# Kernel tuning notes

Measured on AMD Instinct MI355X. Metric: run time of the kernel, lower is better.

## Reference

```python
import jax, jax.numpy as jnp
import numpy as np

B, IN, D, E, K = 16384, 2048, 1024, 3, 2
H1, H2 = 1024, 512


def setup_inputs() -> dict:
    key = jax.random.key(0)
    ks = jax.random.split(key, 10)
    x = jax.random.normal(ks[0], (B, IN), dtype=jnp.float32)
    gate = jax.random.normal(ks[1], (B, E), dtype=jnp.float32)
    topk_probs = jax.random.uniform(ks[2], (B, K), dtype=jnp.float32)
    topk_idx = jax.random.randint(ks[3], (B, K), 0, E)
    s = 0.02
    W1 = jax.random.normal(ks[4], (E, IN, H1), dtype=jnp.float32) * s
    b1 = jnp.zeros((E, H1), dtype=jnp.float32)
    W2 = jax.random.normal(ks[5], (E, H1, H2), dtype=jnp.float32) * s
    b2 = jnp.zeros((E, H2), dtype=jnp.float32)
    W3 = jax.random.normal(ks[6], (E, H2, D), dtype=jnp.float32) * s
    b3 = jnp.zeros((E, D), dtype=jnp.float32)
    return {"x": x, "gate": gate, "topk_probs": topk_probs, "topk_idx": topk_idx,
            "W1": W1, "b1": b1, "W2": W2, "b2": b2, "W3": W3, "b3": b3}


def _lrelu(v):
    return jnp.where(v > 0, v, 0.2 * v)  # LeakyReLU(0.2)


def reference(x, gate, topk_probs, topk_idx, W1, b1, W2, b2, W3, b3):
    # gate is accepted by the original forward but never used.
    n_experts = W1.shape[0]
    # Per-expert 3-layer MLP, batched over experts: [E, B, *]
    h = _lrelu(jnp.einsum('bi,eio->ebo', x, W1) + b1[:, None, :])
    h = _lrelu(jnp.einsum('ebi,eio->ebo', h, W2) + b2[:, None, :])
    y = jnp.einsum('ebi,eio->ebo', h, W3) + b3[:, None, :]  # [E, B, D]
    # Combine: weight for expert e on token b = sum_k probs[b,k] * [idx[b,k]==e]
    onehot = topk_idx[None, :, :] == jnp.arange(n_experts)[:, None, None]  # [E,B,K]
    w = jnp.sum(jnp.where(onehot, topk_probs[None, :, :], 0.0), axis=-1)  # [E,B]
    return jnp.einsum('eb,ebd->bd', w, y)
```

## Files before the change

kernel.cpp:

```cpp
#include <hip/hip_runtime.h>
#include <cstdint>
#include <cstddef>

#define B_TOK   16384
#define IN_DIM  2048
#define D_DIM   1024
#define NEXP    3
#define TOPK    2
#define H1_DIM  1024
#define H2_DIM  512

typedef __bf16 bf16x8 __attribute__((ext_vector_type(8)));
typedef float  f32x4  __attribute__((ext_vector_type(4)));
typedef unsigned short ushort8_t __attribute__((ext_vector_type(8)));

__device__ __forceinline__ unsigned short f2bf(float f) {
    unsigned int u = __builtin_bit_cast(unsigned int, f);
    return (unsigned short)((u + 0x7fffu + ((u >> 16) & 1u)) >> 16);
}
__device__ __forceinline__ float bf2f(unsigned short v) {
    return __builtin_bit_cast(float, (unsigned int)v << 16);
}

__device__ __forceinline__ void glds16(const void* gsrc, void* ldst) {
    __builtin_amdgcn_global_load_lds(
        (__attribute__((address_space(1))) void*)(gsrc),
        (__attribute__((address_space(3))) void*)(ldst),
        16, 0, 0);
}

__global__ __launch_bounds__(256) void prepass(
    const float* __restrict__ x, unsigned short* __restrict__ xb,
    const float* __restrict__ W1s, const float* __restrict__ W2s,
    const float* __restrict__ W3s,
    unsigned short* __restrict__ W1d, unsigned short* __restrict__ W2d,
    unsigned short* __restrict__ W3d,
    const float* __restrict__ probs, const int* __restrict__ tidx,
    int* __restrict__ cnt, int* __restrict__ list, int* __restrict__ inv)
{
    const int bid = blockIdx.x;
    const int t = threadIdx.x;

    if (bid < 2048) {
        const size_t n = (size_t)B_TOK * IN_DIM;
        const size_t stride = (size_t)2048 * 256 * 8;
        size_t i = ((size_t)bid * 256 + t) * 8;
        for (; i < n; i += stride) {
            float4 a = *(const float4*)(x + i);
            float4 b = *(const float4*)(x + i + 4);
            ushort8_t o;
            o[0] = f2bf(a.x); o[1] = f2bf(a.y); o[2] = f2bf(a.z); o[3] = f2bf(a.w);
            o[4] = f2bf(b.x); o[5] = f2bf(b.y); o[6] = f2bf(b.z); o[7] = f2bf(b.w);
            *(ushort8_t*)(xb + i) = o;
        }
    } else if (bid < 4352) {
        __shared__ unsigned short tile[64][68];
        int r = (bid - 2048) % 768;
        int e = (bid - 2048) / 768;
        const float* W; unsigned short* Wt; int K, N, tx;
        if (r < 512)      { W = W1s; Wt = W1d; K = IN_DIM; N = H1_DIM; tx = r; }
        else if (r < 640) { W = W2s; Wt = W2d; K = H1_DIM; N = H2_DIM; tx = r - 512; }
        else              { W = W3s; Wt = W3d; K = H2_DIM; N = D_DIM;  tx = r - 640; }
        const int ntx = N >> 6;
        const float* Wp = W + (size_t)e * K * N;
        unsigned short* Wtp = Wt + (size_t)e * N * K;
        int n0 = (tx % ntx) * 64, k0 = (tx / ntx) * 64;
        int nn = (t & 15) * 4;
        int kk = t >> 4;
        #pragma unroll
        for (int rr = 0; rr < 4; ++rr) {
            int k = kk + rr * 16;
            float4 v = *(const float4*)(Wp + (size_t)(k0 + k) * N + (n0 + nn));
            tile[k][nn + 0] = f2bf(v.x);
            tile[k][nn + 1] = f2bf(v.y);
            tile[k][nn + 2] = f2bf(v.z);
            tile[k][nn + 3] = f2bf(v.w);
        }
        __syncthreads();
        int n  = t >> 2;
        int kb = (t & 3) * 16;
        ushort8_t o0, o1;
        #pragma unroll
        for (int i = 0; i < 8; ++i) o0[i] = tile[kb + i][n];
        #pragma unroll
        for (int i = 0; i < 8; ++i) o1[i] = tile[kb + 8 + i][n];
        unsigned short* dst = Wtp + (size_t)(n0 + n) * K + (k0 + kb);
        *(ushort8_t*)dst = o0;
        *(ushort8_t*)(dst + 8) = o1;
    } else {
        __shared__ int lcnt[NEXP];
        __shared__ int lbase[NEXP];
        __shared__ int ltok[NEXP][256];
        int b = (bid - 4352) * 256 + t;
        if (t < NEXP) lcnt[t] = 0;
        __syncthreads();
        int i0 = tidx[b * TOPK + 0], i1 = tidx[b * TOPK + 1];
        #pragma unroll
        for (int e = 0; e < NEXP; ++e) {
            if (i0 == e || i1 == e) {
                int s = atomicAdd(&lcnt[e], 1);
                ltok[e][s] = b;
            }
        }
        __syncthreads();
        if (t < NEXP) lbase[t] = atomicAdd(&cnt[t], lcnt[t]);
        __syncthreads();
        #pragma unroll
        for (int e = 0; e < NEXP; ++e) {
            int n = lcnt[e], base = lbase[e];
            for (int s = t; s < n; s += 256) {
                int tk = ltok[e][s];
                list[e * B_TOK + base + s] = tk;
                inv[e * B_TOK + tk] = base + s;
            }
        }
    }
}

__global__ __launch_bounds__(256) void combine_out(
    const float* __restrict__ probs, const int* __restrict__ tidx,
    const int* __restrict__ inv, const unsigned short* __restrict__ y, size_t ypl,
    float* __restrict__ out)
{
    int gid = blockIdx.x * 256 + threadIdx.x;
    int tok = gid >> 7;
    int dc  = (gid & 127) << 3;
    float p0 = probs[tok * TOPK + 0], p1 = probs[tok * TOPK + 1];
    int   i0 = tidx [tok * TOPK + 0], i1 = tidx [tok * TOPK + 1];
    size_t r0 = (size_t)i0 * ypl + (size_t)inv[(size_t)i0 * B_TOK + tok] * D_DIM + dc;
    size_t r1 = (size_t)i1 * ypl + (size_t)inv[(size_t)i1 * B_TOK + tok] * D_DIM + dc;
    ushort8_t a = *(const ushort8_t*)(y + r0);
    ushort8_t b = *(const ushort8_t*)(y + r1);
    float4 o0, o1;
    o0.x = p0 * bf2f(a[0]) + p1 * bf2f(b[0]);
    o0.y = p0 * bf2f(a[1]) + p1 * bf2f(b[1]);
    o0.z = p0 * bf2f(a[2]) + p1 * bf2f(b[2]);
    o0.w = p0 * bf2f(a[3]) + p1 * bf2f(b[3]);
    o1.x = p0 * bf2f(a[4]) + p1 * bf2f(b[4]);
    o1.y = p0 * bf2f(a[5]) + p1 * bf2f(b[5]);
    o1.z = p0 * bf2f(a[6]) + p1 * bf2f(b[6]);
    o1.w = p0 * bf2f(a[7]) + p1 * bf2f(b[7]);
    float* op = out + (size_t)tok * D_DIM + dc;
    *(float4*)op = o0;
    *(float4*)(op + 4) = o1;
}

template<int ACT, int GATHER>
__global__ __launch_bounds__(512, 2) void gemm8(
    const unsigned short* __restrict__ Ab, size_t Aplane,
    const unsigned short* __restrict__ Bb,
    const float* __restrict__ biasb,
    unsigned short* __restrict__ Hb,
    size_t plane,
    const int* __restrict__ listb,
    const int* __restrict__ cntb,
    int N, int K, int NT, int e0)
{
    const int bid  = blockIdx.x;
    const int xcd  = bid & 7;
    const int slot = bid >> 3;
    const int q    = slot / NT;
    const int nt   = slot % NT;
    const int ti   = q * 8 + xcd;
    const int e    = e0 + (ti >> 6);
    const int mt   = ti & 63;
    const int bm   = mt << 8;
    const int cp   = (cntb[e] + 255) & ~255;
    if (bm >= cp) return;
    const int bn   = nt << 8;

    __shared__ char smem[131072];

    const int tid  = threadIdx.x;
    const int lane = tid & 63;
    const int w    = tid >> 6;
    const int wl3  = w & 3;
    const int wn1  = w >> 2;
    const int l15  = lane & 15;
    const int ug8  = (((tid & 7) ^ ((tid >> 3) & 7)) << 3);
    const int sw0  = ((((lane >> 4) + 0) ^ (lane & 7)) << 4);
    const int sw1  = ((((lane >> 4) + 4) ^ (lane & 7)) << 4);

    const int* listp = listb + (size_t)e * B_TOK;
    const unsigned short* Ae = Ab + (size_t)e * Aplane;
    const unsigned short* Be = Bb + (size_t)e * ((size_t)N * K);
    const float* biasp = biasb + (size_t)e * N;

    const unsigned short* sA[2][2];
    const unsigned short* sB[2][2];
    #pragma unroll
    for (int h = 0; h < 2; ++h)
        #pragma unroll
        for (int j = 0; j < 2; ++j) {
            int lrow = h * 128 + j * 64 + (tid >> 3);
            int arow;
            if constexpr (GATHER) arow = listp[bm + lrow];
            else                  arow = bm + lrow;
            sA[h][j] = Ae + (size_t)arow * K + ug8;
            sB[h][j] = Be + (size_t)(bn + lrow) * K + ug8;
        }

    char* const stA = smem + (w << 10);
    char* const stB = smem + 65536 + (w << 10);
    const char* const rA = smem + (wl3 * 32 + l15) * 128;
    const char* const rB = smem + 65536 + (wn1 * 64 + l15) * 128;

    f32x4 acc[2][2][2][4] = {};
    bf16x8 av[2][2];
    bf16x8 bv[4][2];

#define STA(db, h, kt) do {                                                     \
    glds16(sA[h][0] + (size_t)(kt) * 64, stA + (db) * 32768 + (h) * 16384);     \
    glds16(sA[h][1] + (size_t)(kt) * 64, stA + (db) * 32768 + (h) * 16384 + 8192); } while (0)
#define STB(db, h, kt) do {                                                     \
    glds16(sB[h][0] + (size_t)(kt) * 64, stB + (db) * 32768 + (h) * 16384);     \
    glds16(sB[h][1] + (size_t)(kt) * 64, stB + (db) * 32768 + (h) * 16384 + 8192); } while (0)

#define LAk(db, Qm, kk) do {                                                    \
    _Pragma("unroll")                                                           \
    for (int ml = 0; ml < 2; ++ml)                                              \
        av[ml][kk] = *(const bf16x8*)(rA + (db)*32768 + (Qm)*16384 + ml*2048    \
                                      + ((kk) ? sw1 : sw0));                    \
    } while (0)
#define LBk(db, Qn, kk) do {                                                    \
    _Pragma("unroll")                                                           \
    for (int nl = 0; nl < 4; ++nl)                                              \
        bv[nl][kk] = *(const bf16x8*)(rB + (db)*32768 + (Qn)*16384 + nl*2048    \
                                      + ((kk) ? sw1 : sw0));                    \
    } while (0)

#define GK(Qm, Qn, kk) do {                                                     \
    _Pragma("unroll")                                                           \
    for (int ml = 0; ml < 2; ++ml)                                              \
        _Pragma("unroll")                                                       \
        for (int nl = 0; nl < 4; ++nl)                                          \
            acc[Qm][ml][Qn][nl] = __builtin_amdgcn_mfma_f32_16x16x32_bf16(      \
                av[ml][kk], bv[nl][kk], acc[Qm][ml][Qn][nl], 0, 0, 0);          \
    } while (0)

#define WINDOW(Qm, Qn, STAGE_STMT, VM_STMT, LK0, LK1) do {                      \
    STAGE_STMT;                                                                 \
    VM_STMT;                                                                    \
    __builtin_amdgcn_s_setprio(1);                                              \
    GK(Qm, Qn, 0);                                                              \
    __builtin_amdgcn_sched_barrier(0);                                          \
    LK0;                                                                        \
    __builtin_amdgcn_sched_barrier(0);                                          \
    GK(Qm, Qn, 1);                                                              \
    __builtin_amdgcn_sched_barrier(0);                                          \
    LK1;                                                                        \
    __builtin_amdgcn_s_setprio(0);                                              \
    __builtin_amdgcn_sched_barrier(0);                                          \
    __builtin_amdgcn_s_barrier();                                               \
} while (0)

    const int nkt = K >> 6;
    STA(0, 0, 0); STA(0, 1, 0); STB(0, 0, 0); STB(0, 1, 0);
    STA(1, 0, 1); STB(1, 0, 1);
    asm volatile("s_waitcnt vmcnt(4)" ::: "memory");
    __builtin_amdgcn_s_barrier();
    LAk(0, 1, 0); LAk(0, 1, 1); LBk(0, 0, 0); LBk(0, 0, 1);

    const int niter = nkt >> 1;
    for (int it = 0; it < niter; ++it) {
        const int t1 = 2 * it + 1;
        const int t2 = (2 * it + 2 < nkt) ? 2 * it + 2 : nkt - 1;
        const int t3 = (2 * it + 3 < nkt) ? 2 * it + 3 : nkt - 1;
        WINDOW(1, 0, STA(1, 1, t1), ((void)0), LAk(0, 0, 0), LAk(0, 0, 1));
        WINDOW(0, 0, STB(1, 1, t1), ((void)0), LBk(0, 1, 0), LBk(0, 1, 1));
        WINDOW(0, 1, STA(0, 0, t2), ((void)0), LAk(0, 1, 0), LAk(0, 1, 1));
        WINDOW(1, 1, STB(0, 0, t2),
               asm volatile("s_waitcnt vmcnt(4)" ::: "memory"),
               LAk(1, 1, 0); LBk(1, 0, 0), LAk(1, 1, 1); LBk(1, 0, 1));
        WINDOW(1, 0, STA(0, 1, t2), ((void)0), LAk(1, 0, 0), LAk(1, 0, 1));
        WINDOW(0, 0, STB(0, 1, t2), ((void)0), LBk(1, 1, 0), LBk(1, 1, 1));
        WINDOW(0, 1, STA(1, 0, t3), ((void)0), LAk(1, 1, 0), LAk(1, 1, 1));
        WINDOW(1, 1, STB(1, 0, t3),
               asm volatile("s_waitcnt vmcnt(4)" ::: "memory"),
               LAk(0, 1, 0); LBk(0, 0, 0), LAk(0, 1, 1); LBk(0, 0, 1));
    }
    asm volatile("s_waitcnt vmcnt(0)" ::: "memory");

    const int rl = (lane >> 4) << 2;
    float bsv[2][4];
    #pragma unroll
    for (int Qn = 0; Qn < 2; ++Qn)
        #pragma unroll
        for (int nl = 0; nl < 4; ++nl)
            bsv[Qn][nl] = biasp[bn + Qn * 128 + wn1 * 64 + nl * 16 + l15];

    unsigned short* Hp = Hb + (size_t)e * plane;
    #pragma unroll
    for (int Qm = 0; Qm < 2; ++Qm)
    #pragma unroll
    for (int ml = 0; ml < 2; ++ml)
    #pragma unroll
    for (int jj = 0; jj < 4; ++jj) {
        int srow = bm + Qm * 128 + wl3 * 32 + ml * 16 + rl + jj;
        size_t ro = (size_t)srow * N;
        #pragma unroll
        for (int Qn = 0; Qn < 2; ++Qn)
        #pragma unroll
        for (int nl = 0; nl < 4; ++nl) {
            int col = bn + Qn * 128 + wn1 * 64 + nl * 16 + l15;
            float v = acc[Qm][ml][Qn][nl][jj] + bsv[Qn][nl];
            if (ACT) v = v > 0.f ? v : 0.2f * v;
            Hp[ro + col] = f2bf(v);
        }
    }
#undef WINDOW
#undef GK
#undef LAk
#undef LBk
#undef STA
#undef STB
}


extern "C" void kernel_launch(void* const* d_in, const int* in_sizes, int n_in,
                              void* d_out, int out_size, void* d_ws, size_t ws_size,
                              hipStream_t stream)
{
    const float* x     = (const float*)d_in[0];
    const float* probs = (const float*)d_in[2];
    const int*   tidx  = (const int*)d_in[3];
    const float* W1    = (const float*)d_in[4];
    const float* b1    = (const float*)d_in[5];
    const float* W2    = (const float*)d_in[6];
    const float* b2    = (const float*)d_in[7];
    const float* W3    = (const float*)d_in[8];
    const float* b3    = (const float*)d_in[9];
    float* out = (float*)d_out;

    char* ws = (char*)d_ws;
    const size_t xb_off  = 0;
    const size_t w1t_off = xb_off  + (size_t)B_TOK * IN_DIM * 2;
    const size_t w2t_off = w1t_off + (size_t)NEXP * IN_DIM * H1_DIM * 2;
    const size_t w3t_off = w2t_off + (size_t)NEXP * H1_DIM * H2_DIM * 2;
    const size_t h1_off  = w3t_off + (size_t)NEXP * H2_DIM * D_DIM * 2;
    const size_t h2_off  = h1_off  + (size_t)NEXP * B_TOK * H1_DIM * 2;
    const size_t y_off   = h2_off  + (size_t)NEXP * B_TOK * H2_DIM * 2;
    const size_t li_off  = y_off   + (size_t)NEXP * B_TOK * D_DIM * 2;
    const size_t cn_off  = li_off  + (size_t)NEXP * B_TOK * 4;
    const size_t iv_off  = cn_off  + 256;

    unsigned short* xb  = (unsigned short*)(ws + xb_off);
    unsigned short* W1t = (unsigned short*)(ws + w1t_off);
    unsigned short* W2t = (unsigned short*)(ws + w2t_off);
    unsigned short* W3t = (unsigned short*)(ws + w3t_off);
    unsigned short* h1  = (unsigned short*)(ws + h1_off);
    unsigned short* h2  = (unsigned short*)(ws + h2_off);
    unsigned short* y   = (unsigned short*)(ws + y_off);
    int*            lst = (int*)(ws + li_off);
    int*            cnt = (int*)(ws + cn_off);
    int*            inv = (int*)(ws + iv_off);

    hipMemsetAsync(lst, 0, (size_t)NEXP * B_TOK * 4 + 256, stream);

    prepass<<<4416, 256, 0, stream>>>(x, xb, W1, W2, W3, W1t, W2t, W3t,
                                      probs, tidx, cnt, lst, inv);

    const size_t h1pl = (size_t)B_TOK * H1_DIM;
    const size_t h2pl = (size_t)B_TOK * H2_DIM;
    const size_t ypl  = (size_t)B_TOK * D_DIM;

    gemm8<1, 1><<<dim3(NEXP * 64 * 4), 512, 0, stream>>>(
        xb, 0, W1t, b1, h1, h1pl,
        lst, cnt, H1_DIM, IN_DIM, 4, 0);
    gemm8<1, 0><<<dim3(NEXP * 64 * 2), 512, 0, stream>>>(
        h1, h1pl, W2t, b2, h2, h2pl,
        lst, cnt, H2_DIM, H1_DIM, 2, 0);
    gemm8<0, 0><<<dim3(NEXP * 64 * 4), 512, 0, stream>>>(
        h2, h2pl, W3t, b3, y, ypl,
        lst, cnt, D_DIM, H2_DIM, 4, 0);
    combine_out<<<dim3(B_TOK * 128 / 256), 256, 0, stream>>>(
        probs, tidx, inv, y, ypl, out);
}
```

Before: 276.6 us.

## Move W2/W3 bf16 transposes from prepass into extra blocks of first GEMM

The prepass now only converts x and W1 and builds the routing lists. The W2 and W3 bf16 transposes run in 384 extra 512-thread blocks appended to the layer-1 GEMM launch, two 256-thread tiles per block. The aim is to shorten the serial prepass and overlap the weight conversion with GEMM1's tail or idle CUs. The cost is that those extra blocks reserve 128KB of shared memory each, so they compete with GEMM tiles for CU slots, and the grid scheduling order decides whether they actually overlap.

```diff
diff --git a/kernel.cpp b/kernel.cpp
--- a/kernel.cpp
+++ b/kernel.cpp
@@ -29,13 +29,38 @@
         16, 0, 0);
 }
 
+__device__ __forceinline__ void transpose_tile_256(
+    const float* __restrict__ Wp, unsigned short* __restrict__ Wtp,
+    int K, int N, int n0, int k0, int t, unsigned short (*tile)[68])
+{
+    int nn = (t & 15) * 4;
+    int kk = t >> 4;
+    #pragma unroll
+    for (int rr = 0; rr < 4; ++rr) {
+        int k = kk + rr * 16;
+        float4 v = *(const float4*)(Wp + (size_t)(k0 + k) * N + (n0 + nn));
+        tile[k][nn + 0] = f2bf(v.x);
+        tile[k][nn + 1] = f2bf(v.y);
+        tile[k][nn + 2] = f2bf(v.z);
+        tile[k][nn + 3] = f2bf(v.w);
+    }
+    __syncthreads();
+    int n  = t >> 2;
+    int kb = (t & 3) * 16;
+    ushort8_t o0, o1;
+    #pragma unroll
+    for (int i = 0; i < 8; ++i) o0[i] = tile[kb + i][n];
+    #pragma unroll
+    for (int i = 0; i < 8; ++i) o1[i] = tile[kb + 8 + i][n];
+    unsigned short* dst = Wtp + (size_t)(n0 + n) * K + (k0 + kb);
+    *(ushort8_t*)dst = o0;
+    *(ushort8_t*)(dst + 8) = o1;
+}
+
 __global__ __launch_bounds__(256) void prepass(
     const float* __restrict__ x, unsigned short* __restrict__ xb,
-    const float* __restrict__ W1s, const float* __restrict__ W2s,
-    const float* __restrict__ W3s,
-    unsigned short* __restrict__ W1d, unsigned short* __restrict__ W2d,
-    unsigned short* __restrict__ W3d,
-    const float* __restrict__ probs, const int* __restrict__ tidx,
+    const float* __restrict__ W1s, unsigned short* __restrict__ W1d,
+    const int* __restrict__ tidx,
     int* __restrict__ cnt, int* __restrict__ list, int* __restrict__ inv)
 {
     const int bid = blockIdx.x;
@@ -53,45 +78,21 @@
             o[4] = f2bf(b.x); o[5] = f2bf(b.y); o[6] = f2bf(b.z); o[7] = f2bf(b.w);
             *(ushort8_t*)(xb + i) = o;
         }
-    } else if (bid < 4352) {
+    } else if (bid < 3584) {
         __shared__ unsigned short tile[64][68];
-        int r = (bid - 2048) % 768;
-        int e = (bid - 2048) / 768;
-        const float* W; unsigned short* Wt; int K, N, tx;
-        if (r < 512)      { W = W1s; Wt = W1d; K = IN_DIM; N = H1_DIM; tx = r; }
-        else if (r < 640) { W = W2s; Wt = W2d; K = H1_DIM; N = H2_DIM; tx = r - 512; }
-        else              { W = W3s; Wt = W3d; K = H2_DIM; N = D_DIM;  tx = r - 640; }
-        const int ntx = N >> 6;
-        const float* Wp = W + (size_t)e * K * N;
-        unsigned short* Wtp = Wt + (size_t)e * N * K;
-        int n0 = (tx % ntx) * 64, k0 = (tx / ntx) * 64;
-        int nn = (t & 15) * 4;
-        int kk = t >> 4;
-        #pragma unroll
-        for (int rr = 0; rr < 4; ++rr) {
-            int k = kk + rr * 16;
-            float4 v = *(const float4*)(Wp + (size_t)(k0 + k) * N + (n0 + nn));
-            tile[k][nn + 0] = f2bf(v.x);
-            tile[k][nn + 1] = f2bf(v.y);
-            tile[k][nn + 2] = f2bf(v.z);
-            tile[k][nn + 3] = f2bf(v.w);
-        }
-        __syncthreads();
-        int n  = t >> 2;
-        int kb = (t & 3) * 16;
-        ushort8_t o0, o1;
-        #pragma unroll
-        for (int i = 0; i < 8; ++i) o0[i] = tile[kb + i][n];
-        #pragma unroll
-        for (int i = 0; i < 8; ++i) o1[i] = tile[kb + 8 + i][n];
-        unsigned short* dst = Wtp + (size_t)(n0 + n) * K + (k0 + kb);
-        *(ushort8_t*)dst = o0;
-        *(ushort8_t*)(dst + 8) = o1;
+        int g = bid - 2048;
+        int e = g / 512;
+        int r = g % 512;
+        const int ntx = H1_DIM >> 6;
+        int n0 = (r % ntx) * 64, k0 = (r / ntx) * 64;
+        transpose_tile_256(W1s + (size_t)e * IN_DIM * H1_DIM,
+                           W1d + (size_t)e * H1_DIM * IN_DIM,
+                           IN_DIM, H1_DIM, n0, k0, t, tile);
     } else {
         __shared__ int lcnt[NEXP];
         __shared__ int lbase[NEXP];
         __shared__ int ltok[NEXP][256];
-        int b = (bid - 4352) * 256 + t;
+        int b = (bid - 3584) * 256 + t;
         if (t < NEXP) lcnt[t] = 0;
         __syncthreads();
         int i0 = tidx[b * TOPK + 0], i1 = tidx[b * TOPK + 1];
@@ -145,7 +146,7 @@
     *(float4*)(op + 4) = o1;
 }
 
-template<int ACT, int GATHER>
+template<int ACT, int GATHER, int XTRA>
 __global__ __launch_bounds__(512, 2) void gemm8(
     const unsigned short* __restrict__ Ab, size_t Aplane,
     const unsigned short* __restrict__ Bb,
@@ -154,9 +155,32 @@
     size_t plane,
     const int* __restrict__ listb,
     const int* __restrict__ cntb,
-    int N, int K, int NT, int e0)
+    int N, int K, int NT, int e0, int NTOT,
+    const float* __restrict__ W2s, const float* __restrict__ W3s,
+    unsigned short* __restrict__ W2d, unsigned short* __restrict__ W3d)
 {
+    __shared__ char smem[131072];
+
     const int bid  = blockIdx.x;
+    const int tid  = threadIdx.x;
+
+    if constexpr (XTRA) {
+        if (bid >= NTOT) {
+            int half = tid >> 8;
+            int t    = tid & 255;
+            int g = (bid - NTOT) * 2 + half;
+            const float* W; unsigned short* Wt; int K2, N2, e, r;
+            if (g < 384) { e = g / 128; r = g % 128; W = W2s; Wt = W2d; K2 = H1_DIM; N2 = H2_DIM; }
+            else { g -= 384; e = g / 128; r = g % 128; W = W3s; Wt = W3d; K2 = H2_DIM; N2 = D_DIM; }
+            const int ntx = N2 >> 6;
+            int n0 = (r % ntx) * 64, k0 = (r / ntx) * 64;
+            unsigned short (*tile)[68] = (unsigned short(*)[68])(smem + half * 8704);
+            transpose_tile_256(W + (size_t)e * K2 * N2, Wt + (size_t)e * N2 * K2,
+                               K2, N2, n0, k0, t, tile);
+            return;
+        }
+    }
+
     const int xcd  = bid & 7;
     const int slot = bid >> 3;
     const int q    = slot / NT;
@@ -169,9 +193,6 @@
     if (bm >= cp) return;
     const int bn   = nt << 8;
 
-    __shared__ char smem[131072];
-
-    const int tid  = threadIdx.x;
     const int lane = tid & 63;
     const int w    = tid >> 6;
     const int wl3  = w & 3;
@@ -357,22 +378,24 @@
 
     hipMemsetAsync(lst, 0, (size_t)NEXP * B_TOK * 4 + 256, stream);
 
-    prepass<<<4416, 256, 0, stream>>>(x, xb, W1, W2, W3, W1t, W2t, W3t,
-                                      probs, tidx, cnt, lst, inv);
+    prepass<<<3648, 256, 0, stream>>>(x, xb, W1, W1t, tidx, cnt, lst, inv);
 
     const size_t h1pl = (size_t)B_TOK * H1_DIM;
     const size_t h2pl = (size_t)B_TOK * H2_DIM;
     const size_t ypl  = (size_t)B_TOK * D_DIM;
 
-    gemm8<1, 1><<<dim3(NEXP * 64 * 4), 512, 0, stream>>>(
+    gemm8<1, 1, 1><<<dim3(NEXP * 64 * 4 + 384), 512, 0, stream>>>(
         xb, 0, W1t, b1, h1, h1pl,
-        lst, cnt, H1_DIM, IN_DIM, 4, 0);
-    gemm8<1, 0><<<dim3(NEXP * 64 * 2), 512, 0, stream>>>(
+        lst, cnt, H1_DIM, IN_DIM, 4, 0, NEXP * 64 * 4,
+        W2, W3, W2t, W3t);
+    gemm8<1, 0, 0><<<dim3(NEXP * 64 * 2), 512, 0, stream>>>(
         h1, h1pl, W2t, b2, h2, h2pl,
-        lst, cnt, H2_DIM, H1_DIM, 2, 0);
-    gemm8<0, 0><<<dim3(NEXP * 64 * 4), 512, 0, stream>>>(
+        lst, cnt, H2_DIM, H1_DIM, 2, 0, NEXP * 64 * 2,
+        nullptr, nullptr, nullptr, nullptr);
+    gemm8<0, 0, 0><<<dim3(NEXP * 64 * 4), 512, 0, stream>>>(
         h2, h2pl, W3t, b3, y, ypl,
-        lst, cnt, D_DIM, H2_DIM, 4, 0);
+        lst, cnt, D_DIM, H2_DIM, 4, 0, NEXP * 64 * 4,
+        nullptr, nullptr, nullptr, nullptr);
     combine_out<<<dim3(B_TOK * 128 / 256), 256, 0, stream>>>(
         probs, tidx, inv, y, ypl, out);
 }
```

Measured after the change: 272.4 us. No clear change (-1.5%).
